# Performance work log

Measured on AMD Instinct MI355X. Metric: run time of the kernel, lower is better.

The kernel has to match this reference:

```python
import jax, jax.numpy as jnp
import numpy as np

B, M, N, D, H = 8, 64, 64, 256, 8

def setup_inputs() -> dict:
    key = jax.random.key(0)
    kx, kq, kk, kv, ko = jax.random.split(key, 5)
    x = jax.random.normal(kx, (B, M, N, D), dtype=jnp.float32)
    q = jax.random.normal(kq, (H, D, D), dtype=jnp.float32)
    k = jax.random.normal(kk, (D, D), dtype=jnp.float32)
    v = jax.random.normal(kv, (D, D), dtype=jnp.float32)
    o = jax.random.normal(ko, (H, D, D), dtype=jnp.float32)
    return {"x": x, "q": q, "k": k, "v": v, "o": o}

def reference(x, q, k, v, o):
    # x: [b,m,n,d]; q,o: [h,d,d]; k,v: [d,d]
    Q = jnp.einsum('bmnd,hdk->bhmnk', x, q)      # [b,h,m,n,d]
    h_half = Q.shape[1] // 2
    Q1, Q2 = Q[:, :h_half], Q[:, h_half:]
    K = jnp.einsum('bmnd,dk->bmnk', x, k)        # [b,m,n,d]
    V = jnp.einsum('bmnd,dv->bmnv', x, v)        # [b,m,n,d]

    # Axis 1: attend along the m (row) axis for each column y
    logits1 = jnp.einsum('bhxyk,bzyk->bhyxz', Q1, K)   # [b,h/2,n,m,m]
    scores1 = jax.nn.softmax(logits1, axis=-1)
    O1 = jnp.einsum('bhyxz,bzyv->bhxyv', scores1, V)   # [b,h/2,m,n,d]

    # Axis 2: attend along the n (column) axis for each row x
    logits2 = jnp.einsum('bhxyk,bxzk->bhxyz', Q2, K)   # [b,h/2,m,n,n]
    scores2 = jax.nn.softmax(logits2, axis=-1)
    O2 = jnp.einsum('bhxyz,bxzv->bhxyv', scores2, V)   # [b,h/2,m,n,d]

    O = jnp.concatenate([O1, O2], axis=1)              # [b,h,m,n,d]
    # Faithful to original: 'bhmnd,hdv->bmnd' keeps d, sums over h and v
    Z = jnp.einsum('bhmnd,hdv->bmnd', O, o)
    return Z
```

## Files before the change

### kernel.cpp

```cpp
#include <hip/hip_runtime.h>

typedef unsigned short u16;
typedef __attribute__((ext_vector_type(8))) short short8;
typedef __attribute__((ext_vector_type(4))) float f32x4;

__device__ __forceinline__ float bf2f(u16 u){ return __uint_as_float(((unsigned)u)<<16); }
__device__ __forceinline__ u16 f2bf(float f){
  unsigned u = __float_as_uint(f);
  unsigned r = u + 0x7fffu + ((u>>16)&1u);
  return (u16)(r>>16);
}

#define MFMA16(a,b,c) __builtin_amdgcn_mfma_f32_16x16x32_bf16(a,b,c,0,0,0)

static constexpr int XS_STR  = 264;
static constexpr int PS_STR  = 72;
static constexpr int WT_STR  = 72;
static constexpr int XHI_OFF = 0;
static constexpr int XLO_OFF = 16896;
static constexpr int GT_OFF  = 33792;
static constexpr int XVT_OFF = 50688;
static constexpr int PS_OFF  = 69120;
static constexpr int SMRE_OFF= 73728;
static constexpr int SMEM_BYTES = (73728 + 512)*2;

static constexpr int MH_SMEM = 22016*2;


__global__ void prep_kernel(const float* __restrict__ k, const float* __restrict__ v,
                            const float* __restrict__ o, u16* __restrict__ khi,
                            u16* __restrict__ klo, u16* __restrict__ vT,
                            float* __restrict__ soP, float4* __restrict__ outz){
  __shared__ float Ts[64*65];
  const int blk = blockIdx.x, tid = threadIdx.x;
  if (blk < 64){
    int base = blk*1024 + tid*4;
    const float4 f4 = *(const float4*)(k + base);
    ushort4 hv, lv;
    hv.x=f2bf(f4.x); lv.x=f2bf(f4.x-bf2f(hv.x));
    hv.y=f2bf(f4.y); lv.y=f2bf(f4.y-bf2f(hv.y));
    hv.z=f2bf(f4.z); lv.z=f2bf(f4.z-bf2f(hv.z));
    hv.w=f2bf(f4.w); lv.w=f2bf(f4.w-bf2f(hv.w));
    *(ushort4*)&khi[base] = hv;
    *(ushort4*)&klo[base] = lv;
  } else if (blk < 80){
    int t = blk - 64;
    const int bi = (t>>2)<<6, bj = (t&3)<<6;
    #pragma unroll
    for (int p=0;p<4;p++){
      int idx4 = tid + (p<<8);
      int i = idx4 >> 4, c4 = (idx4 & 15) << 2;
      const float4 f4 = *(const float4*)(v + ((bi+i)<<8) + bj + c4);
      Ts[i*65+c4]=f4.x; Ts[i*65+c4+1]=f4.y; Ts[i*65+c4+2]=f4.z; Ts[i*65+c4+3]=f4.w;
    }
    __syncthreads();
    #pragma unroll
    for (int p=0;p<2;p++){
      int ch = tid + (p<<8);
      int j = ch >> 3, i8 = (ch & 7) << 3;
      short8 t8;
      #pragma unroll
      for (int e=0;e<8;e++) t8[e] = (short)f2bf(Ts[(i8+e)*65 + j]);
      *(short8*)&vT[((bj+j)<<8) + bi + i8] = t8;
    }
  } else if (blk < 336){
    int p = blk - 80;
    int h = p >> 5, base = (p & 31) << 3;
    int w = tid >> 6, l = tid & 63;
    #pragma unroll
    for (int i=0;i<2;i++){
      int row = base + w*2 + i;
      const float4 f4 = *(const float4*)(o + (((h<<8)+row)<<8) + (l<<2));
      float s = f4.x + f4.y + f4.z + f4.w;
      #pragma unroll
      for (int off=32; off>=1; off>>=1) s += __shfl_xor(s, off, 64);
      if (l==0) soP[(h<<8)+row] = s;
    }
  } else {
    int z = blk - 336;
    const float4 zf4 = {0.f,0.f,0.f,0.f};
    #pragma unroll
    for (int i=0;i<16;i++) outz[z*4096 + i*256 + tid] = zf4;
  }
}

__global__ __launch_bounds__(256,1) void mh_kernel(
    const float* __restrict__ q, const u16* __restrict__ khi,
    const u16* __restrict__ klo, u16* __restrict__ mhi, u16* __restrict__ mlo)
{
  extern __shared__ u16 sm[];
  u16* Qhi = sm;
  u16* Qlo = sm + 8448;
  u16* Chi = sm + 16896;
  u16* Clo = sm + 19456;

  const int tid = threadIdx.x;
  const int w = tid >> 6, lane = tid & 63;
  const int quad = lane >> 4, m16 = lane & 15;
  const int cw2 = w << 4, koq = quad << 3;
  const int h   = blockIdx.x >> 5;
  const int rr  = blockIdx.x & 31;
  const int dt  = (rr >> 2) << 5;
  const int dpq = (rr & 3) << 6;

  #pragma unroll
  for (int i=0;i<8;i++){
    int idx4 = i*256 + tid;
    int tr = idx4 >> 6, c4 = (idx4 & 63) << 2;
    const float4 xv = *(const float4*)(q + (((h<<8)+dt+tr)<<8) + c4);
    ushort4 hv, lv;
    hv.x=f2bf(xv.x); lv.x=f2bf(xv.x-bf2f(hv.x));
    hv.y=f2bf(xv.y); lv.y=f2bf(xv.y-bf2f(hv.y));
    hv.z=f2bf(xv.z); lv.z=f2bf(xv.z-bf2f(hv.z));
    hv.w=f2bf(xv.w); lv.w=f2bf(xv.w-bf2f(hv.w));
    *(ushort4*)&Qhi[tr*XS_STR + c4] = hv;
    *(ushort4*)&Qlo[tr*XS_STR + c4] = lv;
  }
  __syncthreads();

  const f32x4 zf = {0.f,0.f,0.f,0.f};
  f32x4 a0 = zf, a1 = zf;
  #pragma unroll
  for (int kk=0;kk<8;kk++){
    const int ko = (kk<<5) + koq;
    short8 Ah0 = *(const short8*)&Qhi[(m16)*XS_STR + ko];
    short8 Al0 = *(const short8*)&Qlo[(m16)*XS_STR + ko];
    short8 Ah1 = *(const short8*)&Qhi[(16+m16)*XS_STR + ko];
    short8 Al1 = *(const short8*)&Qlo[(16+m16)*XS_STR + ko];
    short8 Bh  = *(const short8*)&khi[(dpq+cw2+m16)*256 + ko];
    short8 Bl  = *(const short8*)&klo[(dpq+cw2+m16)*256 + ko];
    a0 = MFMA16(Ah0,Bh,a0); a0 = MFMA16(Ah0,Bl,a0); a0 = MFMA16(Al0,Bh,a0);
    a1 = MFMA16(Ah1,Bh,a1); a1 = MFMA16(Ah1,Bl,a1); a1 = MFMA16(Al1,Bh,a1);
  }

  const int dpl = cw2 + m16;
  #pragma unroll
  for (int g=0; g<4; g++){
    float v0 = a0[g]; u16 h0 = f2bf(v0);
    Chi[dpl*40 + quad*4+g] = h0;
    Clo[dpl*40 + quad*4+g] = f2bf(v0 - bf2f(h0));
    float v1 = a1[g]; u16 h1 = f2bf(v1);
    Chi[dpl*40 + 16 + quad*4+g] = h1;
    Clo[dpl*40 + 16 + quad*4+g] = f2bf(v1 - bf2f(h1));
  }
  __syncthreads();

  int dpo = tid >> 2, i8 = (tid & 3) << 3;
  *(int4*)&mhi[(((h<<8)+dpq+dpo)<<8) + dt + i8] = *(const int4*)&Chi[dpo*40 + i8];
  *(int4*)&mlo[(((h<<8)+dpq+dpo)<<8) + dt + i8] = *(const int4*)&Clo[dpo*40 + i8];
}

__global__ __launch_bounds__(512,2) void attn_kernel(
    const float* __restrict__ x, const u16* __restrict__ mhiP,
    const u16* __restrict__ mloP, const u16* __restrict__ vT,
    const float* __restrict__ soP, float* __restrict__ out)
{
  extern __shared__ u16 sm[];
  u16* Xhi = sm + XHI_OFF;
  u16* Xlo = sm + XLO_OFF;
  u16* Gt  = sm + GT_OFF;
  u16* Xvt = sm + XVT_OFF;
  u16* Ps  = sm + PS_OFF;
  float* SMf = (float*)(sm + SMRE_OFF);

  const int tid  = threadIdx.x;
  const int w    = tid >> 6, lane = tid & 63;
  const int quad = lane >> 4, m16 = lane & 15;
  const int br   = blockIdx.x >> 9;
  const int idx  = blockIdx.x & 511;
  const int b    = idx >> 6, s = idx & 63;
  const int cw   = w << 5;
  const int rs   = (w >> 1) << 4;
  const int zh   = w & 1;
  const int koq  = quad << 3;

  auto tok = [&](int t)->int {
    int m = br ? s : t;
    int n = br ? t : s;
    return (((b<<6) + m) << 14) + (n << 8);
  };

  #pragma unroll
  for (int i=0;i<8;i++){
    int idx4 = i*512 + tid;
    int tr = idx4 >> 6, c4 = (idx4 & 63) << 2;
    const float4 xv = *(const float4*)(x + tok(tr) + c4);
    ushort4 hv, lv;
    hv.x=f2bf(xv.x); lv.x=f2bf(xv.x-bf2f(hv.x));
    hv.y=f2bf(xv.y); lv.y=f2bf(xv.y-bf2f(hv.y));
    hv.z=f2bf(xv.z); lv.z=f2bf(xv.z-bf2f(hv.z));
    hv.w=f2bf(xv.w); lv.w=f2bf(xv.w-bf2f(hv.w));
    *(ushort4*)&Xhi[tr*XS_STR + c4] = hv;
    *(ushort4*)&Xlo[tr*XS_STR + c4] = lv;
  }
  __syncthreads();

  short8 XB[16];
  #pragma unroll
  for (int kk=0;kk<8;kk++)
    #pragma unroll
    for (int c=0;c<2;c++)
      XB[kk*2+c] = *(const short8*)&Xhi[((zh<<5) + c*16 + m16)*XS_STR + (kk<<5) + koq];

  const f32x4 zf = {0.f,0.f,0.f,0.f};
  f32x4 acc[4][2];

  auto mm3 = [&](const u16* __restrict__ Whi, const u16* __restrict__ Wlo){
    #pragma unroll
    for (int r=0;r<4;r++){ acc[r][0] = zf; acc[r][1] = zf; }
    short8 Bh[2][2], Bl[2][2];
    #pragma unroll
    for (int c=0;c<2;c++){
      Bh[0][c] = *(const short8*)&Whi[(cw + c*16 + m16)*256 + koq];
      Bl[0][c] = *(const short8*)&Wlo[(cw + c*16 + m16)*256 + koq];
    }
    #pragma unroll
    for (int kk=0;kk<8;kk++){
      const int cur = kk&1, nxt = cur^1;
      if (kk<7){
        const int ko2 = ((kk+1)<<5) + koq;
        #pragma unroll
        for (int c=0;c<2;c++){
          Bh[nxt][c] = *(const short8*)&Whi[(cw + c*16 + m16)*256 + ko2];
          Bl[nxt][c] = *(const short8*)&Wlo[(cw + c*16 + m16)*256 + ko2];
        }
      }
      const int ko = (kk<<5) + koq;
      short8 Ah[4], Al[4];
      #pragma unroll
      for (int r=0;r<4;r++) Ah[r] = *(const short8*)&Xhi[(r*16+m16)*XS_STR + ko];
      #pragma unroll
      for (int r=0;r<4;r++) Al[r] = *(const short8*)&Xlo[(r*16+m16)*XS_STR + ko];
      #pragma unroll
      for (int r=0;r<4;r++)
        #pragma unroll
        for (int c=0;c<2;c++){
          acc[r][c] = MFMA16(Ah[r], Bh[cur][c], acc[r][c]);
          acc[r][c] = MFMA16(Ah[r], Bl[cur][c], acc[r][c]);
          acc[r][c] = MFMA16(Al[r], Bh[cur][c], acc[r][c]);
        }
    }
  };

  {
    #pragma unroll
    for (int r=0;r<4;r++){ acc[r][0] = zf; acc[r][1] = zf; }
    #pragma unroll
    for (int kk=0;kk<8;kk++){
      const int ko = (kk<<5) + koq;
      short8 A[4], Bf[2];
      #pragma unroll
      for (int r=0;r<4;r++) A[r]  = *(const short8*)&Xhi[(r*16+m16)*XS_STR + ko];
      #pragma unroll
      for (int c=0;c<2;c++) Bf[c] = *(const short8*)&vT[(cw + c*16 + m16)*256 + ko];
      #pragma unroll
      for (int r=0;r<4;r++)
        #pragma unroll
        for (int c=0;c<2;c++) acc[r][c] = MFMA16(A[r], Bf[c], acc[r][c]);
    }
    #pragma unroll
    for (int r=0;r<4;r++)
      #pragma unroll
      for (int c=0;c<2;c++)
        #pragma unroll
        for (int g=0; g<4; g++){
          int z  = r*16 + quad*4 + g;
          int vc = cw + c*16 + m16;
          Xvt[vc*WT_STR + z] = f2bf(acc[r][c][g]);
        }
  }

  f32x4 Z[4][2];
  #pragma unroll
  for (int r=0;r<4;r++){ Z[r][0] = zf; Z[r][1] = zf; }

  for (int h=0; h<4; h++){
    const int gh = br*4 + h;

    mm3(mhiP + gh*65536, mloP + gh*65536);
    #pragma unroll
    for (int r=0;r<4;r++)
      #pragma unroll
      for (int c=0;c<2;c++)
        #pragma unroll
        for (int g=0; g<4; g++){
          int row = r*16 + quad*4 + g;
          int col = cw + c*16 + m16;
          Gt[row*XS_STR + col] = f2bf(acc[r][c][g]);
        }
    __syncthreads();

    f32x4 L[2];
    L[0] = zf; L[1] = zf;
    #pragma unroll
    for (int kk=0;kk<8;kk++){
      const int ko = (kk<<5) + koq;
      short8 A = *(const short8*)&Gt[(rs+m16)*XS_STR + ko];
      #pragma unroll
      for (int c=0;c<2;c++){
        L[c] = MFMA16(A, XB[kk*2+c], L[c]);
        short8 Bl = *(const short8*)&Xlo[((zh<<5) + c*16 + m16)*XS_STR + ko];
        L[c] = MFMA16(A, Bl, L[c]);
      }
    }
    __syncthreads();
    #pragma unroll
    for (int r=0;r<4;r++)
      #pragma unroll
      for (int c=0;c<2;c++)
        #pragma unroll
        for (int g=0; g<4; g++){
          int row = r*16 + quad*4 + g;
          int col = cw + c*16 + m16;
          float vv = acc[r][c][g];
          u16 hh = f2bf(vv);
          Gt[row*XS_STR + col] = f2bf(vv - bf2f(hh));
        }
    __syncthreads();

    #pragma unroll
    for (int kk=0;kk<8;kk++){
      const int ko = (kk<<5) + koq;
      short8 A = *(const short8*)&Gt[(rs+m16)*XS_STR + ko];
      #pragma unroll
      for (int c=0;c<2;c++)
        L[c] = MFMA16(A, XB[kk*2+c], L[c]);
    }

    float mxl[4], sml[4];
    #pragma unroll
    for (int g=0; g<4; g++){
      float mx = fmaxf(L[0][g], L[1][g]);
      #pragma unroll
      for (int off=1; off<16; off<<=1) mx = fmaxf(mx, __shfl_xor(mx, off, 64));
      float sum = 0.f;
      #pragma unroll
      for (int c=0;c<2;c++){ float e = __expf(L[c][g]-mx); L[c][g] = e; sum += e; }
      #pragma unroll
      for (int off=1; off<16; off<<=1) sum += __shfl_xor(sum, off, 64);
      mxl[g] = mx; sml[g] = sum;
      if (m16 == 0){
        int row = rs + quad*4 + g;
        SMf[row*4 + zh*2]     = mx;
        SMf[row*4 + zh*2 + 1] = sum;
      }
    }
    __syncthreads();
    #pragma unroll
    for (int g=0; g<4; g++){
      int row = rs + quad*4 + g;
      float mxo = SMf[row*4 + (zh^1)*2];
      float smo = SMf[row*4 + (zh^1)*2 + 1];
      float M   = fmaxf(mxl[g], mxo);
      float al  = __expf(mxl[g]-M), ao = __expf(mxo-M);
      float scale = al / (sml[g]*al + smo*ao);
      #pragma unroll
      for (int c=0;c<2;c++)
        Ps[row*PS_STR + (zh<<5) + c*16 + m16] = f2bf(L[c][g]*scale);
    }
    __syncthreads();

    #pragma unroll
    for (int r=0;r<4;r++){ acc[r][0] = zf; acc[r][1] = zf; }
    #pragma unroll
    for (int kk=0;kk<2;kk++){
      const int ko = (kk<<5) + koq;
      short8 A[4], Bf[2];
      #pragma unroll
      for (int r=0;r<4;r++) A[r]  = *(const short8*)&Ps[(r*16+m16)*PS_STR + ko];
      #pragma unroll
      for (int c=0;c<2;c++) Bf[c] = *(const short8*)&Xvt[(cw + c*16 + m16)*WT_STR + ko];
      #pragma unroll
      for (int r=0;r<4;r++)
        #pragma unroll
        for (int c=0;c<2;c++) acc[r][c] = MFMA16(A[r], Bf[c], acc[r][c]);
    }
    float sc[2];
    sc[0] = soP[gh*256 + cw + m16];
    sc[1] = soP[gh*256 + cw + 16 + m16];
    #pragma unroll
    for (int r=0;r<4;r++)
      #pragma unroll
      for (int c=0;c<2;c++)
        #pragma unroll
        for (int g=0; g<4; g++) Z[r][c][g] += sc[c]*acc[r][c][g];
  }

  #pragma unroll
  for (int r=0;r<4;r++)
    #pragma unroll
    for (int c=0;c<2;c++)
      #pragma unroll
      for (int g=0; g<4; g++){
        int t   = r*16 + quad*4 + g;
        int col = cw + c*16 + m16;
        atomicAdd(&out[tok(t) + col], Z[r][c][g]);
      }
}

extern "C" void kernel_launch(void* const* d_in, const int* in_sizes, int n_in,
                              void* d_out, int out_size, void* d_ws, size_t ws_size,
                              hipStream_t stream) {
  const float* x = (const float*)d_in[0];
  const float* q = (const float*)d_in[1];
  const float* k = (const float*)d_in[2];
  const float* v = (const float*)d_in[3];
  const float* o = (const float*)d_in[4];
  u16* ws   = (u16*)d_ws;
  u16* mhi  = ws;
  u16* mlo  = ws + 524288;
  u16* khi  = ws + 1048576;
  u16* klo  = ws + 1114112;
  u16* vT   = ws + 1179648;
  float* soP = (float*)(ws + 1245184);
  float* out = (float*)d_out;

  prep_kernel<<<848, 256, 0, stream>>>(k, v, o, khi, klo, vT, soP, (float4*)d_out);
  (void)hipFuncSetAttribute(reinterpret_cast<const void*>(&mh_kernel),
                            hipFuncAttributeMaxDynamicSharedMemorySize, MH_SMEM);
  mh_kernel<<<256, 256, MH_SMEM, stream>>>(q, khi, klo, mhi, mlo);

  (void)hipFuncSetAttribute(reinterpret_cast<const void*>(&attn_kernel),
                            hipFuncAttributeMaxDynamicSharedMemorySize, SMEM_BYTES);
  attn_kernel<<<1024, 512, SMEM_BYTES, stream>>>(x, mhi, mlo, vT, soP, out);
}
```

Baseline: 335.5 us.

## Fuse prep and Q·K precompute kernels; add MFMA priority hints in attention

Merges the prep kernel and the mh kernel into one launch. K is now split into bf16 hi/lo in registers inside the mh blocks rather than staged through a workspace buffer, which removes one kernel launch and its dependency barrier. The trade-off is that every mh block redundantly converts its K slice, and the fused kernel's large dynamic LDS allocation with launch_bounds(256,1) also applies to the lightweight prep blocks, which may lower their occupancy. Separately, attention MFMA sequences are wrapped in s_setprio raise/lower so waves issuing matrix ops get scheduling priority, and the Xlo loads are hoisted ahead of the MFMAs.

```diff
diff --git a/kernel.cpp b/kernel.cpp
--- a/kernel.cpp
+++ b/kernel.cpp
@@ -27,24 +27,89 @@
 static constexpr int MH_SMEM = 22016*2;
 
 
-__global__ void prep_kernel(const float* __restrict__ k, const float* __restrict__ v,
-                            const float* __restrict__ o, u16* __restrict__ khi,
-                            u16* __restrict__ klo, u16* __restrict__ vT,
-                            float* __restrict__ soP, float4* __restrict__ outz){
-  __shared__ float Ts[64*65];
+__global__ __launch_bounds__(256,1) void prep_mh_kernel(
+    const float* __restrict__ q, const float* __restrict__ k,
+    const float* __restrict__ v, const float* __restrict__ o,
+    u16* __restrict__ mhi, u16* __restrict__ mlo, u16* __restrict__ vT,
+    float* __restrict__ soP, float4* __restrict__ outz)
+{
+  extern __shared__ u16 sm[];
   const int blk = blockIdx.x, tid = threadIdx.x;
-  if (blk < 64){
-    int base = blk*1024 + tid*4;
-    const float4 f4 = *(const float4*)(k + base);
-    ushort4 hv, lv;
-    hv.x=f2bf(f4.x); lv.x=f2bf(f4.x-bf2f(hv.x));
-    hv.y=f2bf(f4.y); lv.y=f2bf(f4.y-bf2f(hv.y));
-    hv.z=f2bf(f4.z); lv.z=f2bf(f4.z-bf2f(hv.z));
-    hv.w=f2bf(f4.w); lv.w=f2bf(f4.w-bf2f(hv.w));
-    *(ushort4*)&khi[base] = hv;
-    *(ushort4*)&klo[base] = lv;
-  } else if (blk < 80){
-    int t = blk - 64;
+
+  if (blk < 256){
+    u16* Qhi = sm;
+    u16* Qlo = sm + 8448;
+    u16* Chi = sm + 16896;
+    u16* Clo = sm + 19456;
+
+    const int w = tid >> 6, lane = tid & 63;
+    const int quad = lane >> 4, m16 = lane & 15;
+    const int cw2 = w << 4, koq = quad << 3;
+    const int h   = blk >> 5;
+    const int rr  = blk & 31;
+    const int dt  = (rr >> 2) << 5;
+    const int dpq = (rr & 3) << 6;
+
+    #pragma unroll
+    for (int i=0;i<8;i++){
+      int idx4 = i*256 + tid;
+      int tr = idx4 >> 6, c4 = (idx4 & 63) << 2;
+      const float4 xv = *(const float4*)(q + (((h<<8)+dt+tr)<<8) + c4);
+      ushort4 hv, lv;
+      hv.x=f2bf(xv.x); lv.x=f2bf(xv.x-bf2f(hv.x));
+      hv.y=f2bf(xv.y); lv.y=f2bf(xv.y-bf2f(hv.y));
+      hv.z=f2bf(xv.z); lv.z=f2bf(xv.z-bf2f(hv.z));
+      hv.w=f2bf(xv.w); lv.w=f2bf(xv.w-bf2f(hv.w));
+      *(ushort4*)&Qhi[tr*XS_STR + c4] = hv;
+      *(ushort4*)&Qlo[tr*XS_STR + c4] = lv;
+    }
+    __syncthreads();
+
+    const float* kptr = k + (dpq+cw2+m16)*256;
+    const f32x4 zf = {0.f,0.f,0.f,0.f};
+    f32x4 a0 = zf, a1 = zf;
+    #pragma unroll
+    for (int kk=0;kk<8;kk++){
+      const int ko = (kk<<5) + koq;
+      short8 Ah0 = *(const short8*)&Qhi[(m16)*XS_STR + ko];
+      short8 Al0 = *(const short8*)&Qlo[(m16)*XS_STR + ko];
+      short8 Ah1 = *(const short8*)&Qhi[(16+m16)*XS_STR + ko];
+      short8 Al1 = *(const short8*)&Qlo[(16+m16)*XS_STR + ko];
+      short8 Bh, Bl;
+      {
+        const float4 f0 = *(const float4*)(kptr + ko);
+        const float4 f1 = *(const float4*)(kptr + ko + 4);
+        float fv[8] = {f0.x,f0.y,f0.z,f0.w,f1.x,f1.y,f1.z,f1.w};
+        #pragma unroll
+        for (int e=0;e<8;e++){
+          u16 hh = f2bf(fv[e]);
+          Bh[e] = (short)hh;
+          Bl[e] = (short)f2bf(fv[e]-bf2f(hh));
+        }
+      }
+      a0 = MFMA16(Ah0,Bh,a0); a0 = MFMA16(Ah0,Bl,a0); a0 = MFMA16(Al0,Bh,a0);
+      a1 = MFMA16(Ah1,Bh,a1); a1 = MFMA16(Ah1,Bl,a1); a1 = MFMA16(Al1,Bh,a1);
+    }
+
+    const int dpl = cw2 + m16;
+    #pragma unroll
+    for (int g=0; g<4; g++){
+      float v0 = a0[g]; u16 h0 = f2bf(v0);
+      Chi[dpl*40 + quad*4+g] = h0;
+      Clo[dpl*40 + quad*4+g] = f2bf(v0 - bf2f(h0));
+      float v1 = a1[g]; u16 h1 = f2bf(v1);
+      Chi[dpl*40 + 16 + quad*4+g] = h1;
+      Clo[dpl*40 + 16 + quad*4+g] = f2bf(v1 - bf2f(h1));
+    }
+    __syncthreads();
+
+    int dpo = tid >> 2, i8 = (tid & 3) << 3;
+    *(int4*)&mhi[(((h<<8)+dpq+dpo)<<8) + dt + i8] = *(const int4*)&Chi[dpo*40 + i8];
+    *(int4*)&mlo[(((h<<8)+dpq+dpo)<<8) + dt + i8] = *(const int4*)&Clo[dpo*40 + i8];
+
+  } else if (blk < 272){
+    float* Ts = (float*)sm;
+    int t = blk - 256;
     const int bi = (t>>2)<<6, bj = (t&3)<<6;
     #pragma unroll
     for (int p=0;p<4;p++){
@@ -63,8 +128,8 @@
       for (int e=0;e<8;e++) t8[e] = (short)f2bf(Ts[(i8+e)*65 + j]);
       *(short8*)&vT[((bj+j)<<8) + bi + i8] = t8;
     }
-  } else if (blk < 336){
-    int p = blk - 80;
+  } else if (blk < 528){
+    int p = blk - 272;
     int h = p >> 5, base = (p & 31) << 3;
     int w = tid >> 6, l = tid & 63;
     #pragma unroll
@@ -77,77 +142,11 @@
       if (l==0) soP[(h<<8)+row] = s;
     }
   } else {
-    int z = blk - 336;
+    int z = blk - 528;
     const float4 zf4 = {0.f,0.f,0.f,0.f};
     #pragma unroll
     for (int i=0;i<16;i++) outz[z*4096 + i*256 + tid] = zf4;
   }
-}
-
-__global__ __launch_bounds__(256,1) void mh_kernel(
-    const float* __restrict__ q, const u16* __restrict__ khi,
-    const u16* __restrict__ klo, u16* __restrict__ mhi, u16* __restrict__ mlo)
-{
-  extern __shared__ u16 sm[];
-  u16* Qhi = sm;
-  u16* Qlo = sm + 8448;
-  u16* Chi = sm + 16896;
-  u16* Clo = sm + 19456;
-
-  const int tid = threadIdx.x;
-  const int w = tid >> 6, lane = tid & 63;
-  const int quad = lane >> 4, m16 = lane & 15;
-  const int cw2 = w << 4, koq = quad << 3;
-  const int h   = blockIdx.x >> 5;
-  const int rr  = blockIdx.x & 31;
-  const int dt  = (rr >> 2) << 5;
-  const int dpq = (rr & 3) << 6;
-
-  #pragma unroll
-  for (int i=0;i<8;i++){
-    int idx4 = i*256 + tid;
-    int tr = idx4 >> 6, c4 = (idx4 & 63) << 2;
-    const float4 xv = *(const float4*)(q + (((h<<8)+dt+tr)<<8) + c4);
-    ushort4 hv, lv;
-    hv.x=f2bf(xv.x); lv.x=f2bf(xv.x-bf2f(hv.x));
-    hv.y=f2bf(xv.y); lv.y=f2bf(xv.y-bf2f(hv.y));
-    hv.z=f2bf(xv.z); lv.z=f2bf(xv.z-bf2f(hv.z));
-    hv.w=f2bf(xv.w); lv.w=f2bf(xv.w-bf2f(hv.w));
-    *(ushort4*)&Qhi[tr*XS_STR + c4] = hv;
-    *(ushort4*)&Qlo[tr*XS_STR + c4] = lv;
-  }
-  __syncthreads();
-
-  const f32x4 zf = {0.f,0.f,0.f,0.f};
-  f32x4 a0 = zf, a1 = zf;
-  #pragma unroll
-  for (int kk=0;kk<8;kk++){
-    const int ko = (kk<<5) + koq;
-    short8 Ah0 = *(const short8*)&Qhi[(m16)*XS_STR + ko];
-    short8 Al0 = *(const short8*)&Qlo[(m16)*XS_STR + ko];
-    short8 Ah1 = *(const short8*)&Qhi[(16+m16)*XS_STR + ko];
-    short8 Al1 = *(const short8*)&Qlo[(16+m16)*XS_STR + ko];
-    short8 Bh  = *(const short8*)&khi[(dpq+cw2+m16)*256 + ko];
-    short8 Bl  = *(const short8*)&klo[(dpq+cw2+m16)*256 + ko];
-    a0 = MFMA16(Ah0,Bh,a0); a0 = MFMA16(Ah0,Bl,a0); a0 = MFMA16(Al0,Bh,a0);
-    a1 = MFMA16(Ah1,Bh,a1); a1 = MFMA16(Ah1,Bl,a1); a1 = MFMA16(Al1,Bh,a1);
-  }
-
-  const int dpl = cw2 + m16;
-  #pragma unroll
-  for (int g=0; g<4; g++){
-    float v0 = a0[g]; u16 h0 = f2bf(v0);
-    Chi[dpl*40 + quad*4+g] = h0;
-    Clo[dpl*40 + quad*4+g] = f2bf(v0 - bf2f(h0));
-    float v1 = a1[g]; u16 h1 = f2bf(v1);
-    Chi[dpl*40 + 16 + quad*4+g] = h1;
-    Clo[dpl*40 + 16 + quad*4+g] = f2bf(v1 - bf2f(h1));
-  }
-  __syncthreads();
-
-  int dpo = tid >> 2, i8 = (tid & 3) << 3;
-  *(int4*)&mhi[(((h<<8)+dpq+dpo)<<8) + dt + i8] = *(const int4*)&Chi[dpo*40 + i8];
-  *(int4*)&mlo[(((h<<8)+dpq+dpo)<<8) + dt + i8] = *(const int4*)&Clo[dpo*40 + i8];
 }
 
 __global__ __launch_bounds__(512,2) void attn_kernel(
@@ -231,6 +230,7 @@
       for (int r=0;r<4;r++) Ah[r] = *(const short8*)&Xhi[(r*16+m16)*XS_STR + ko];
       #pragma unroll
       for (int r=0;r<4;r++) Al[r] = *(const short8*)&Xlo[(r*16+m16)*XS_STR + ko];
+      __builtin_amdgcn_s_setprio(1);
       #pragma unroll
       for (int r=0;r<4;r++)
         #pragma unroll
@@ -239,6 +239,7 @@
           acc[r][c] = MFMA16(Ah[r], Bl[cur][c], acc[r][c]);
           acc[r][c] = MFMA16(Al[r], Bh[cur][c], acc[r][c]);
         }
+      __builtin_amdgcn_s_setprio(0);
     }
   };
 
@@ -296,12 +297,14 @@
     for (int kk=0;kk<8;kk++){
       const int ko = (kk<<5) + koq;
       short8 A = *(const short8*)&Gt[(rs+m16)*XS_STR + ko];
-      #pragma unroll
-      for (int c=0;c<2;c++){
-        L[c] = MFMA16(A, XB[kk*2+c], L[c]);
-        short8 Bl = *(const short8*)&Xlo[((zh<<5) + c*16 + m16)*XS_STR + ko];
-        L[c] = MFMA16(A, Bl, L[c]);
-      }
+      short8 Bl0 = *(const short8*)&Xlo[((zh<<5) + m16)*XS_STR + ko];
+      short8 Bl1 = *(const short8*)&Xlo[((zh<<5) + 16 + m16)*XS_STR + ko];
+      __builtin_amdgcn_s_setprio(1);
+      L[0] = MFMA16(A, XB[kk*2+0], L[0]);
+      L[0] = MFMA16(A, Bl0, L[0]);
+      L[1] = MFMA16(A, XB[kk*2+1], L[1]);
+      L[1] = MFMA16(A, Bl1, L[1]);
+      __builtin_amdgcn_s_setprio(0);
     }
     __syncthreads();
     #pragma unroll
@@ -322,9 +325,10 @@
     for (int kk=0;kk<8;kk++){
       const int ko = (kk<<5) + koq;
       short8 A = *(const short8*)&Gt[(rs+m16)*XS_STR + ko];
-      #pragma unroll
-      for (int c=0;c<2;c++)
-        L[c] = MFMA16(A, XB[kk*2+c], L[c]);
+      __builtin_amdgcn_s_setprio(1);
+      L[0] = MFMA16(A, XB[kk*2+0], L[0]);
+      L[1] = MFMA16(A, XB[kk*2+1], L[1]);
+      __builtin_amdgcn_s_setprio(0);
     }
 
     float mxl[4], sml[4];
@@ -409,16 +413,14 @@
   u16* ws   = (u16*)d_ws;
   u16* mhi  = ws;
   u16* mlo  = ws + 524288;
-  u16* khi  = ws + 1048576;
-  u16* klo  = ws + 1114112;
   u16* vT   = ws + 1179648;
   float* soP = (float*)(ws + 1245184);
   float* out = (float*)d_out;
 
-  prep_kernel<<<848, 256, 0, stream>>>(k, v, o, khi, klo, vT, soP, (float4*)d_out);
-  (void)hipFuncSetAttribute(reinterpret_cast<const void*>(&mh_kernel),
+  (void)hipFuncSetAttribute(reinterpret_cast<const void*>(&prep_mh_kernel),
                             hipFuncAttributeMaxDynamicSharedMemorySize, MH_SMEM);
-  mh_kernel<<<256, 256, MH_SMEM, stream>>>(q, khi, klo, mhi, mlo);
+  prep_mh_kernel<<<1040, 256, MH_SMEM, stream>>>(q, k, v, o, mhi, mlo, vT, soP,
+                                                 (float4*)d_out);
 
   (void)hipFuncSetAttribute(reinterpret_cast<const void*>(&attn_kernel),
                             hipFuncAttributeMaxDynamicSharedMemorySize, SMEM_BYTES);
```

Result: no change. 331.9 us (-1.1%).
